# Optimization experiments

Hardware: AMD Instinct MI355X
Metric: run time of the kernel (lower is better)

## Reference

```python
import jax, jax.numpy as jnp
import numpy as np
import math

D = 1024; H = 16; DH = 64; L = 4; DFF = 4096; V = 32000; S = 1024; B = 2
EPS = 1e-5

def _pe(seq_len, d):
    pos = jnp.arange(seq_len, dtype=jnp.float32)[:, None]
    div = jnp.exp(jnp.arange(0, d, 2, dtype=jnp.float32) * (-math.log(10000.0) / d))
    pe = jnp.zeros((seq_len, d), jnp.float32)
    pe = pe.at[:, 0::2].set(jnp.sin(pos * div))
    pe = pe.at[:, 1::2].set(jnp.cos(pos * div))
    return pe

def _ln(x, s, b):
    m = jnp.mean(x, -1, keepdims=True)
    v = jnp.var(x, -1, keepdims=True)
    return (x - m) / jnp.sqrt(v + EPS) * s + b

def setup_inputs() -> dict:
    key = jax.random.key(0)
    ks = jax.random.split(key, 12)
    def rn(k, shape, scale=0.02):
        return jax.random.normal(k, shape, jnp.float32) * scale
    return {
        "idx": jax.random.randint(ks[0], (B, S), 0, V),
        "emb": rn(ks[1], (V, D)),                 # tied token-embedding / classifier weight
        "cls_b": jnp.zeros((V,), jnp.float32),
        "ln1_s": jnp.ones((L, D), jnp.float32), "ln1_b": jnp.zeros((L, D), jnp.float32),
        "wq": rn(ks[2], (L, H, D, DH)), "bq": jnp.zeros((L, H, DH), jnp.float32),
        "wk": rn(ks[3], (L, H, D, DH)), "bk": jnp.zeros((L, H, DH), jnp.float32),
        "wv": rn(ks[4], (L, H, D, DH)), "bv": jnp.zeros((L, H, DH), jnp.float32),
        "wo": rn(ks[5], (L, D, D)), "bo": jnp.zeros((L, D), jnp.float32),
        "ln2_s": jnp.ones((L, D), jnp.float32), "ln2_b": jnp.zeros((L, D), jnp.float32),
        "w1": rn(ks[6], (L, D, DFF)), "b1": jnp.zeros((L, DFF), jnp.float32),
        "w2": rn(ks[7], (L, DFF, D)), "b2": jnp.zeros((L, D), jnp.float32),
        "lnf_s": jnp.ones((D,), jnp.float32), "lnf_b": jnp.zeros((D,), jnp.float32),
    }

def reference(idx, emb, cls_b, ln1_s, ln1_b, wq, bq, wk, bk, wv, bv, wo, bo,
              ln2_s, ln2_b, w1, b1, w2, b2, lnf_s, lnf_b):
    b, s = idx.shape
    x = emb[idx] * math.sqrt(D) + _pe(s, D)[None]          # [B,S,D]
    causal = jnp.tril(jnp.ones((s, s), bool))
    scale = 1.0 / math.sqrt(DH)
    for l in range(L):
        h = _ln(x, ln1_s[l], ln1_b[l])
        # all heads at once (same math as per-head loop with separate Linears)
        q = jnp.einsum('bsd,hde->bhse', h, wq[l]) + bq[l][None, :, None, :]
        k = jnp.einsum('bsd,hde->bhse', h, wk[l]) + bk[l][None, :, None, :]
        v = jnp.einsum('bsd,hde->bhse', h, wv[l]) + bv[l][None, :, None, :]
        sc = jnp.einsum('bhse,bhte->bhst', q, k) * scale
        sc = jnp.where(causal[None, None], sc, -jnp.inf)
        w = jax.nn.softmax(sc, axis=-1)
        o = jnp.einsum('bhst,bhte->bhse', w, v)            # [B,H,S,DH]
        o = o.transpose(0, 2, 1, 3).reshape(b, s, D)       # concat heads
        x = x + o @ wo[l] + bo[l]
        h2 = _ln(x, ln2_s[l], ln2_b[l])
        x = x + jax.nn.relu(h2 @ w1[l] + b1[l]) @ w2[l] + b2[l]
    x = _ln(x, lnf_s, lnf_b)
    logits = x @ emb.T + cls_b                              # tied classifier
    return logits
```

## Files before the change

kernel.cpp:

```cpp
#include <hip/hip_runtime.h>
#include <hip/hip_bf16.h>

#define DMODEL 1024
#define NHEAD 16
#define DHEAD 64
#define NLAYER 4
#define DFF_ 4096
#define VOCAB 32000
#define SEQ 1024
#define BATCH 2
#define MTOK (BATCH*SEQ)

typedef __bf16 bf16x8 __attribute__((ext_vector_type(8)));
typedef __bf16 bf16x4v __attribute__((ext_vector_type(4)));
typedef float f32x4 __attribute__((ext_vector_type(4)));
using bf16 = __hip_bfloat16;

__device__ __forceinline__ void async_copy16(const void* g, void* l) {
  __builtin_amdgcn_global_load_lds(
      (__attribute__((address_space(1))) void*)(g),
      (__attribute__((address_space(3))) void*)(l),
      16, 0, 0);
}


__global__ __launch_bounds__(256) void convert_bf16_kernel(
    const float* __restrict__ in, bf16* __restrict__ out, long n) {
  long i = ((long)blockIdx.x * 256 + threadIdx.x) * 4;
  if (i >= n) return;
  float4 v = *(const float4*)(in + i);
  bf16x4v p;
  p[0] = (__bf16)v.x; p[1] = (__bf16)v.y; p[2] = (__bf16)v.z; p[3] = (__bf16)v.w;
  *(bf16x4v*)((__bf16*)out + i) = p;
}

__global__ void transpose_cvt(const float* __restrict__ in, bf16* __restrict__ out,
                              int R, int C, long inBatchStride, int subB,
                              long outStrideL, long outStrideH, long outOff) {
  __shared__ float tile[32][33];
  int bi = blockIdx.z;
  int l = bi / subB, h = bi - l * subB;
  const float* src = in + (size_t)bi * inBatchStride;
  bf16* dst = out + (size_t)l * outStrideL + (size_t)h * outStrideH + outOff;
  int r0 = blockIdx.y * 32, c0 = blockIdx.x * 32;
#pragma unroll
  for (int k = 0; k < 4; k++)
    tile[threadIdx.y + 8 * k][threadIdx.x] =
        src[(size_t)(r0 + threadIdx.y + 8 * k) * C + c0 + threadIdx.x];
  __syncthreads();
#pragma unroll
  for (int k = 0; k < 4; k++)
    dst[(size_t)(c0 + threadIdx.y + 8 * k) * R + r0 + threadIdx.x] =
        __float2bfloat16(tile[threadIdx.x][threadIdx.y + 8 * k]);
}

__global__ __launch_bounds__(256) void pack_qkv_bias(
    const float* __restrict__ bq, const float* __restrict__ bk,
    const float* __restrict__ bv, float* __restrict__ outb) {
  int i = blockIdx.x * 256 + threadIdx.x;
  if (i >= NLAYER * 3072) return;
  int l = i / 3072, r = i - l * 3072;
  int seg = r >> 10, n = r & 1023;
  const float* src = (seg == 0) ? bq : (seg == 1 ? bk : bv);
  outb[i] = src[l * 1024 + n];
}


__global__ __launch_bounds__(256) void embed_kernel(
    const int* __restrict__ idx, const float* __restrict__ emb, float* __restrict__ x) {
  int row = blockIdx.x;
  int s = row & (SEQ - 1);
  int token = idx[row];
  const float* e = emb + (size_t)token * DMODEL;
  float* xr = x + (size_t)row * DMODEL;
  int c = threadIdx.x * 4;
  float4 v = *(const float4*)(e + c);
  float o[4];
  const float vv[4] = {v.x, v.y, v.z, v.w};
#pragma unroll
  for (int u = 0; u < 4; u++) {
    int cc = c + u;
    int ii = cc >> 1;
    float div = expf((float)(2 * ii) * (-9.210340371976184f / 1024.f));
    float arg = (float)s * div;
    float pe = (cc & 1) ? cosf(arg) : sinf(arg);
    o[u] = vv[u] * 32.0f + pe;
  }
  *(float4*)(xr + c) = *(float4*)o;
}


__global__ __launch_bounds__(256) void ln_kernel(
    const float* __restrict__ x, const float* __restrict__ gs,
    const float* __restrict__ gb, bf16* __restrict__ out) {
  int row = blockIdx.x;
  const float* xr = x + (size_t)row * DMODEL;
  int c = threadIdx.x * 4;
  float4 v = *(const float4*)(xr + c);
  float s = v.x + v.y + v.z + v.w;
  float s2 = v.x * v.x + v.y * v.y + v.z * v.z + v.w * v.w;
#pragma unroll
  for (int off = 1; off < 64; off <<= 1) {
    s  += __shfl_xor(s, off, 64);
    s2 += __shfl_xor(s2, off, 64);
  }
  __shared__ float ps[4], ps2[4];
  int wave = threadIdx.x >> 6, lane = threadIdx.x & 63;
  if (lane == 0) { ps[wave] = s; ps2[wave] = s2; }
  __syncthreads();
  float ts = ps[0] + ps[1] + ps[2] + ps[3];
  float ts2 = ps2[0] + ps2[1] + ps2[2] + ps2[3];
  float mean = ts * (1.f / DMODEL);
  float var = ts2 * (1.f / DMODEL) - mean * mean;
  float rstd = rsqrtf(var + 1e-5f);
  const float vv[4] = {v.x, v.y, v.z, v.w};
  bf16x4v p;
#pragma unroll
  for (int u = 0; u < 4; u++) {
    float val = (vv[u] - mean) * rstd * gs[c + u] + gb[c + u];
    p[u] = (__bf16)val;
  }
  *(bf16x4v*)((__bf16*)out + (size_t)row * DMODEL + c) = p;
}


template <int OUTBF, int RELU, int RESID, int BN>
__global__ __launch_bounds__(256) void gemm_bt(
    const bf16* __restrict__ A, const bf16* __restrict__ Wt,
    const float* __restrict__ bias, const float* __restrict__ resid,
    void* __restrict__ out, int M, int N, int K) {
  constexpr int NJ = BN / 32;
  __shared__ bf16 As[2][128 * 32];
  __shared__ bf16 Bs[2][BN * 32];
  const int tid = threadIdx.x;
  const int wave = tid >> 6, lane = tid & 63;
  const int lrow = lane & 15, quad = lane >> 4;
  const int wr = wave >> 1, wc = wave & 1;

  const int nbm = M >> 7;
  const int nbn = N / BN;
  const int nwg = nbm * nbn;
  const int xcd = blockIdx.x & 7, local = blockIdx.x >> 3;
  const int q8 = nwg >> 3, r8 = nwg & 7;
  const int swz = (xcd < r8 ? xcd * (q8 + 1) : r8 * (q8 + 1) + (xcd - r8) * q8) + local;
  const int tm = (swz % nbm) * 128;
  const int tn = (swz / nbm) * BN;

  f32x4 acc[4][NJ] = {};

  auto STAGE = [&](int buf, int k0) {
#pragma unroll
    for (int j = 0; j < 2; j++) {
      int c = j * 256 + tid;
      int row = c >> 2, cp = c & 3;
      const bf16* ga = A + (size_t)(tm + row) * K + k0 + cp * 8;
      async_copy16(ga, (void*)(As[buf] + (j * 256 + wave * 64) * 8));
    }
#pragma unroll
    for (int j = 0; j < NJ / 2; j++) {
      int c = j * 256 + tid;
      int row = c >> 2, cp = c & 3;
      const bf16* gb = Wt + (size_t)(tn + row) * K + k0 + cp * 8;
      async_copy16(gb, (void*)(Bs[buf] + (j * 256 + wave * 64) * 8));
    }
  };

  STAGE(0, 0);
  __syncthreads();

  const int nk = K >> 5;
  int cur = 0;
  for (int kt = 0; kt < nk; ++kt) {
    if (kt + 1 < nk) STAGE(cur ^ 1, (kt + 1) << 5);
    bf16x8 af[4], bfr[NJ];
#pragma unroll
    for (int i = 0; i < 4; i++)
      af[i] = *(const bf16x8*)(As[cur] + (wr * 64 + i * 16 + lrow) * 32 + quad * 8);
#pragma unroll
    for (int j = 0; j < NJ; j++)
      bfr[j] = *(const bf16x8*)(Bs[cur] + (wc * (NJ * 16) + j * 16 + lrow) * 32 + quad * 8);
#pragma unroll
    for (int i = 0; i < 4; i++)
#pragma unroll
      for (int j = 0; j < NJ; j++)
        acc[i][j] = __builtin_amdgcn_mfma_f32_16x16x32_bf16(af[i], bfr[j], acc[i][j], 0, 0, 0);
    __syncthreads();
    cur ^= 1;
  }

#pragma unroll
  for (int i = 0; i < 4; i++) {
#pragma unroll
    for (int j = 0; j < NJ; j++) {
#pragma unroll
      for (int r = 0; r < 4; r++) {
        int grow = tm + wr * 64 + i * 16 + quad * 4 + r;
        int gcol = tn + wc * (NJ * 16) + j * 16 + lrow;
        float v = acc[i][j][r];
        if (bias) v += bias[gcol];
        if (RESID) v += resid[(size_t)grow * N + gcol];
        if (RELU) v = fmaxf(v, 0.f);
        if (OUTBF) ((bf16*)out)[(size_t)grow * N + gcol] = __float2bfloat16(v);
        else       ((float*)out)[(size_t)grow * N + gcol] = v;
      }
    }
  }
}


__global__ __launch_bounds__(256) void attn_kernel(
    const bf16* __restrict__ qkv, bf16* __restrict__ o) {
  __shared__ bf16 Qs[64 * 64];
  __shared__ bf16 Ks[64 * 64];
  __shared__ bf16 Vt[64 * 64];
  __shared__ bf16 Ps[64 * 64];
  int qt = blockIdx.x;
  int bh = blockIdx.y;
  int b = bh >> 4, h = bh & 15;
  int tid = threadIdx.x;
  int wave = tid >> 6, lane = tid & 63;
  int lrow = lane & 15, quad = lane >> 4;
  const size_t rs = 3072;
  const bf16* qb = qkv + ((size_t)b * SEQ + qt * 64) * rs + h * 64;
#pragma unroll
  for (int j = 0; j < 2; j++) {
    int c = j * 256 + tid;
    int r = c >> 3, cp = c & 7;
    *(uint4*)((__bf16*)Qs + r * 64 + cp * 8) = *(const uint4*)((const __bf16*)qb + (size_t)r * rs + cp * 8);
  }
  float m_i[4], l_i[4];
  f32x4 acc_o[4] = {};
#pragma unroll
  for (int r = 0; r < 4; r++) { m_i[r] = -1e30f; l_i[r] = 0.f; }

  for (int kt = 0; kt <= qt; kt++) {
    const bf16* kb = qkv + ((size_t)b * SEQ + kt * 64) * rs + 1024 + h * 64;
    const bf16* vb = qkv + ((size_t)b * SEQ + kt * 64) * rs + 2048 + h * 64;
    __syncthreads();
#pragma unroll
    for (int j = 0; j < 2; j++) {
      int c = j * 256 + tid;
      int r = c >> 3, cp = c & 7;
      *(uint4*)((__bf16*)Ks + r * 64 + cp * 8) = *(const uint4*)((const __bf16*)kb + (size_t)r * rs + cp * 8);
      uint4 vv = *(const uint4*)((const __bf16*)vb + (size_t)r * rs + cp * 8);
      const bf16* ve = (const bf16*)&vv;
#pragma unroll
      for (int e = 0; e < 8; e++) Vt[(cp * 8 + e) * 64 + r] = ve[e];
    }
    __syncthreads();
    f32x4 sc[4] = {};
#pragma unroll
    for (int ks = 0; ks < 2; ks++) {
      bf16x8 aq = *(const bf16x8*)((__bf16*)Qs + (wave * 16 + lrow) * 64 + ks * 32 + quad * 8);
#pragma unroll
      for (int j = 0; j < 4; j++) {
        bf16x8 bk = *(const bf16x8*)((__bf16*)Ks + (j * 16 + lrow) * 64 + ks * 32 + quad * 8);
        sc[j] = __builtin_amdgcn_mfma_f32_16x16x32_bf16(aq, bk, sc[j], 0, 0, 0);
      }
    }
    int grow_base = qt * 64 + wave * 16 + quad * 4;
    bool diag = (kt == qt);
#pragma unroll
    for (int r = 0; r < 4; r++) {
      int grow = grow_base + r;
      float mx = -1e30f;
#pragma unroll
      for (int j = 0; j < 4; j++) {
        float v = sc[j][r] * 0.125f;
        if (diag) { int gcol = kt * 64 + j * 16 + lrow; if (gcol > grow) v = -1e30f; }
        sc[j][r] = v;
        mx = fmaxf(mx, v);
      }
#pragma unroll
      for (int off = 1; off < 16; off <<= 1) mx = fmaxf(mx, __shfl_xor(mx, off, 64));
      float mnew = fmaxf(m_i[r], mx);
      float alpha = __expf(m_i[r] - mnew);
      float rsum = 0.f;
#pragma unroll
      for (int j = 0; j < 4; j++) {
        float p = __expf(sc[j][r] - mnew);
        sc[j][r] = p;
        rsum += p;
      }
#pragma unroll
      for (int off = 1; off < 16; off <<= 1) rsum += __shfl_xor(rsum, off, 64);
      l_i[r] = l_i[r] * alpha + rsum;
      m_i[r] = mnew;
#pragma unroll
      for (int j = 0; j < 4; j++) acc_o[j][r] *= alpha;
    }
#pragma unroll
    for (int j = 0; j < 4; j++)
#pragma unroll
      for (int r = 0; r < 4; r++)
        Ps[(wave * 16 + quad * 4 + r) * 64 + j * 16 + lrow] = __float2bfloat16(sc[j][r]);
    __syncthreads();
#pragma unroll
    for (int ks = 0; ks < 2; ks++) {
      bf16x8 ap = *(const bf16x8*)((__bf16*)Ps + (wave * 16 + lrow) * 64 + ks * 32 + quad * 8);
#pragma unroll
      for (int j = 0; j < 4; j++) {
        bf16x8 bv = *(const bf16x8*)((__bf16*)Vt + (j * 16 + lrow) * 64 + ks * 32 + quad * 8);
        acc_o[j] = __builtin_amdgcn_mfma_f32_16x16x32_bf16(ap, bv, acc_o[j], 0, 0, 0);
      }
    }
  }
#pragma unroll
  for (int r = 0; r < 4; r++) {
    float inv = 1.f / l_i[r];
    int grow = qt * 64 + wave * 16 + quad * 4 + r;
#pragma unroll
    for (int j = 0; j < 4; j++) {
      int e = j * 16 + lrow;
      o[((size_t)b * SEQ + grow) * DMODEL + h * 64 + e] = __float2bfloat16(acc_o[j][r] * inv);
    }
  }
}


extern "C" void kernel_launch(void* const* d_in, const int* in_sizes, int n_in,
                              void* d_out, int out_size, void* d_ws, size_t ws_size,
                              hipStream_t stream) {
  const int*   idx   = (const int*)d_in[0];
  const float* emb   = (const float*)d_in[1];
  const float* cls_b = (const float*)d_in[2];
  const float* ln1_s = (const float*)d_in[3];
  const float* ln1_b = (const float*)d_in[4];
  const float* wq    = (const float*)d_in[5];
  const float* bq    = (const float*)d_in[6];
  const float* wk    = (const float*)d_in[7];
  const float* bk    = (const float*)d_in[8];
  const float* wv    = (const float*)d_in[9];
  const float* bv    = (const float*)d_in[10];
  const float* wo    = (const float*)d_in[11];
  const float* bo    = (const float*)d_in[12];
  const float* ln2_s = (const float*)d_in[13];
  const float* ln2_b = (const float*)d_in[14];
  const float* w1    = (const float*)d_in[15];
  const float* b1    = (const float*)d_in[16];
  const float* w2    = (const float*)d_in[17];
  const float* b2    = (const float*)d_in[18];
  const float* lnf_s = (const float*)d_in[19];
  const float* lnf_b = (const float*)d_in[20];
  float* out = (float*)d_out;

  char* ws = (char*)d_ws;
  bf16* emb_bf = (bf16*)ws;  ws += (size_t)VOCAB * DMODEL * 2;
  bf16* wqkv_t = (bf16*)ws;  ws += (size_t)NLAYER * 3072 * 1024 * 2;
  float* bqkv  = (float*)ws; ws += (size_t)NLAYER * 3072 * 4;
  bf16* wo_t   = (bf16*)ws;  ws += (size_t)NLAYER * 1024 * 1024 * 2;
  bf16* w1_t   = (bf16*)ws;  ws += (size_t)NLAYER * 4096 * 1024 * 2;
  bf16* w2_t   = (bf16*)ws;  ws += (size_t)NLAYER * 1024 * 4096 * 2;
  float* x     = (float*)ws; ws += (size_t)MTOK * DMODEL * 4;
  bf16* hbuf   = (bf16*)ws;  ws += (size_t)MTOK * DMODEL * 2;
  bf16* qkvb   = (bf16*)ws;  ws += (size_t)MTOK * 3072 * 2;
  bf16* obuf   = (bf16*)ws;  ws += (size_t)MTOK * DMODEL * 2;
  bf16* midb   = (bf16*)ws;  ws += (size_t)MTOK * DFF_ * 2;

  convert_bf16_kernel<<<(VOCAB * DMODEL) / 1024, 256, 0, stream>>>(emb, emb_bf, (long)VOCAB * DMODEL);
  dim3 tb(32, 8);
  for (int sel = 0; sel < 3; sel++) {
    const float* src = (sel == 0) ? wq : (sel == 1 ? wk : wv);
    transpose_cvt<<<dim3(64 / 32, 1024 / 32, NLAYER * NHEAD), tb, 0, stream>>>(
        src, wqkv_t, 1024, 64, (long)1024 * 64, NHEAD,
        (long)3072 * 1024, (long)64 * 1024, (long)sel * 1024 * 1024);
  }
  pack_qkv_bias<<<(NLAYER * 3072 + 255) / 256, 256, 0, stream>>>(bq, bk, bv, bqkv);
  transpose_cvt<<<dim3(1024 / 32, 1024 / 32, NLAYER), tb, 0, stream>>>(
      wo, wo_t, 1024, 1024, (long)1024 * 1024, 1, (long)1024 * 1024, 0, 0);
  transpose_cvt<<<dim3(4096 / 32, 1024 / 32, NLAYER), tb, 0, stream>>>(
      w1, w1_t, 1024, 4096, (long)1024 * 4096, 1, (long)4096 * 1024, 0, 0);
  transpose_cvt<<<dim3(1024 / 32, 4096 / 32, NLAYER), tb, 0, stream>>>(
      w2, w2_t, 4096, 1024, (long)4096 * 1024, 1, (long)1024 * 4096, 0, 0);

  embed_kernel<<<MTOK, 256, 0, stream>>>(idx, emb, x);

  const int nbm = MTOK / 128;
  for (int l = 0; l < NLAYER; l++) {
    ln_kernel<<<MTOK, 256, 0, stream>>>(x, ln1_s + l * 1024, ln1_b + l * 1024, hbuf);
    gemm_bt<1, 0, 0, 128><<<dim3(nbm * (3072 / 128)), 256, 0, stream>>>(
        hbuf, wqkv_t + (size_t)l * 3072 * 1024, bqkv + l * 3072, nullptr, qkvb, MTOK, 3072, 1024);
    attn_kernel<<<dim3(SEQ / 64, BATCH * NHEAD), 256, 0, stream>>>(qkvb, obuf);
    gemm_bt<0, 0, 1, 64><<<dim3(nbm * (1024 / 64)), 256, 0, stream>>>(
        obuf, wo_t + (size_t)l * 1024 * 1024, bo + l * 1024, x, x, MTOK, 1024, 1024);
    ln_kernel<<<MTOK, 256, 0, stream>>>(x, ln2_s + l * 1024, ln2_b + l * 1024, hbuf);
    gemm_bt<1, 1, 0, 128><<<dim3(nbm * (4096 / 128)), 256, 0, stream>>>(
        hbuf, w1_t + (size_t)l * 4096 * 1024, b1 + l * 4096, nullptr, midb, MTOK, 4096, 1024);
    gemm_bt<0, 0, 1, 64><<<dim3(nbm * (1024 / 64)), 256, 0, stream>>>(
        midb, w2_t + (size_t)l * 1024 * 4096, b2 + l * 1024, x, x, MTOK, 1024, 4096);
  }
  ln_kernel<<<MTOK, 256, 0, stream>>>(x, lnf_s, lnf_b, hbuf);
  gemm_bt<0, 0, 0, 128><<<dim3(nbm * (VOCAB / 128)), 256, 0, stream>>>(
      hbuf, emb_bf, cls_b, nullptr, out, MTOK, VOCAB, 1024);
}
```

Baseline: 1.711 ms.

## Add 256x128-tile GEMM with XCD swizzle for QKV, FFN1 and classifier

Introduces a new GEMM kernel with 256x128 output tiles (8x4 MFMA accumulators per wave), async global-to-LDS double buffering, and s_setprio around the MFMA block. Block indices are remapped across the 8 XCDs so neighbouring tiles land on the same XCD's L2. It is used for the wide-N GEMMs (QKV, FFN up, vocab projection) to raise arithmetic intensity per loaded tile and improve cache locality. Higher register pressure (128 accumulator floats) may limit occupancy, and the grid shrinks for smaller GEMMs.

```diff
diff --git a/kernel.cpp b/kernel.cpp
--- a/kernel.cpp
+++ b/kernel.cpp
@@ -196,6 +196,87 @@
       for (int r = 0; r < 4; r++) {
         int grow = tm + wr * 64 + i * 16 + quad * 4 + r;
         int gcol = tn + wc * (NJ * 16) + j * 16 + lrow;
+        float v = acc[i][j][r];
+        if (bias) v += bias[gcol];
+        if (RESID) v += resid[(size_t)grow * N + gcol];
+        if (RELU) v = fmaxf(v, 0.f);
+        if (OUTBF) ((bf16*)out)[(size_t)grow * N + gcol] = __float2bfloat16(v);
+        else       ((float*)out)[(size_t)grow * N + gcol] = v;
+      }
+    }
+  }
+}
+
+
+template <int OUTBF, int RELU, int RESID>
+__global__ __launch_bounds__(256, 2) void gemm256(
+    const bf16* __restrict__ A, const bf16* __restrict__ Wt,
+    const float* __restrict__ bias, const float* __restrict__ resid,
+    void* __restrict__ out, int M, int N, int K) {
+  __shared__ bf16 As[2][256 * 32];
+  __shared__ bf16 Bs[2][128 * 32];
+  const int tid = threadIdx.x;
+  const int wave = tid >> 6, lane = tid & 63;
+  const int lrow = lane & 15, quad = lane >> 4;
+  const int wr = wave >> 1, wc = wave & 1;
+
+  const int nbm = M >> 8;
+  const int nbn = N >> 7;
+  const int nwg = nbm * nbn;
+  const int xcd = blockIdx.x & 7, local = blockIdx.x >> 3;
+  const int q8 = nwg >> 3, r8 = nwg & 7;
+  const int swz = (xcd < r8 ? xcd * (q8 + 1) : r8 * (q8 + 1) + (xcd - r8) * q8) + local;
+  const int tm = (swz % nbm) * 256;
+  const int tn = (swz / nbm) * 128;
+
+  f32x4 acc[8][4] = {};
+
+  const int arow = tid >> 2;
+  const int acol = (tid & 3) * 8;
+  auto STAGE = [&](int buf, int k0) {
+    const bf16* ga = A + (size_t)(tm + arow) * K + k0 + acol;
+#pragma unroll
+    for (int ci = 0; ci < 4; ci++)
+      async_copy16(ga + (size_t)ci * 64 * K, (void*)(As[buf] + ci * 2048 + tid * 8));
+    const bf16* gb = Wt + (size_t)(tn + arow) * K + k0 + acol;
+#pragma unroll
+    for (int ci = 0; ci < 2; ci++)
+      async_copy16(gb + (size_t)ci * 64 * K, (void*)(Bs[buf] + ci * 2048 + tid * 8));
+  };
+
+  STAGE(0, 0);
+  STAGE(1, 32);
+  __syncthreads();
+
+  const int nk = K >> 5;
+  for (int t = 0; t < nk; ++t) {
+    const int cur = t & 1;
+    bf16x8 af[8], bfr[4];
+#pragma unroll
+    for (int i = 0; i < 8; i++)
+      af[i] = *(const bf16x8*)(As[cur] + (wr * 128 + i * 16 + lrow) * 32 + quad * 8);
+#pragma unroll
+    for (int j = 0; j < 4; j++)
+      bfr[j] = *(const bf16x8*)(Bs[cur] + (wc * 64 + j * 16 + lrow) * 32 + quad * 8);
+    __builtin_amdgcn_s_setprio(1);
+#pragma unroll
+    for (int i = 0; i < 8; i++)
+#pragma unroll
+      for (int j = 0; j < 4; j++)
+        acc[i][j] = __builtin_amdgcn_mfma_f32_16x16x32_bf16(af[i], bfr[j], acc[i][j], 0, 0, 0);
+    __builtin_amdgcn_s_setprio(0);
+    __syncthreads();
+    if (t + 2 < nk) STAGE(cur, (t + 2) << 5);
+  }
+
+#pragma unroll
+  for (int i = 0; i < 8; i++) {
+#pragma unroll
+    for (int j = 0; j < 4; j++) {
+#pragma unroll
+      for (int r = 0; r < 4; r++) {
+        int grow = tm + wr * 128 + i * 16 + quad * 4 + r;
+        int gcol = tn + wc * 64 + j * 16 + lrow;
         float v = acc[i][j][r];
         if (bias) v += bias[gcol];
         if (RESID) v += resid[(size_t)grow * N + gcol];
@@ -376,20 +457,21 @@
   embed_kernel<<<MTOK, 256, 0, stream>>>(idx, emb, x);
 
   const int nbm = MTOK / 128;
+  const int nbm256 = MTOK / 256;
   for (int l = 0; l < NLAYER; l++) {
     ln_kernel<<<MTOK, 256, 0, stream>>>(x, ln1_s + l * 1024, ln1_b + l * 1024, hbuf);
-    gemm_bt<1, 0, 0, 128><<<dim3(nbm * (3072 / 128)), 256, 0, stream>>>(
+    gemm256<1, 0, 0><<<dim3(nbm256 * (3072 / 128)), 256, 0, stream>>>(
         hbuf, wqkv_t + (size_t)l * 3072 * 1024, bqkv + l * 3072, nullptr, qkvb, MTOK, 3072, 1024);
     attn_kernel<<<dim3(SEQ / 64, BATCH * NHEAD), 256, 0, stream>>>(qkvb, obuf);
     gemm_bt<0, 0, 1, 64><<<dim3(nbm * (1024 / 64)), 256, 0, stream>>>(
         obuf, wo_t + (size_t)l * 1024 * 1024, bo + l * 1024, x, x, MTOK, 1024, 1024);
     ln_kernel<<<MTOK, 256, 0, stream>>>(x, ln2_s + l * 1024, ln2_b + l * 1024, hbuf);
-    gemm_bt<1, 1, 0, 128><<<dim3(nbm * (4096 / 128)), 256, 0, stream>>>(
+    gemm256<1, 1, 0><<<dim3(nbm256 * (4096 / 128)), 256, 0, stream>>>(
         hbuf, w1_t + (size_t)l * 4096 * 1024, b1 + l * 4096, nullptr, midb, MTOK, 4096, 1024);
     gemm_bt<0, 0, 1, 64><<<dim3(nbm * (1024 / 64)), 256, 0, stream>>>(
         midb, w2_t + (size_t)l * 1024 * 4096, b2 + l * 1024, x, x, MTOK, 1024, 4096);
   }
   ln_kernel<<<MTOK, 256, 0, stream>>>(x, lnf_s, lnf_b, hbuf);
-  gemm_bt<0, 0, 0, 128><<<dim3(nbm * (VOCAB / 128)), 256, 0, stream>>>(
+  gemm256<0, 0, 0><<<dim3(nbm256 * (VOCAB / 128)), 256, 0, stream>>>(
       hbuf, emb_bf, cls_b, nullptr, out, MTOK, VOCAB, 1024);
 }
```

Result: slower. 1.793 ms (+4.8%).
